# Kernel optimization log

Hardware: AMD Instinct MI355X
Metric: run time of the kernel (lower is better)

The kernel has to match this reference:

```python
import jax, jax.numpy as jnp
import numpy as np

EPSILON = 1e-06
N_TOKENS = 65536
WIDTH_IN = 1024
WIDTH_OUT = 1024
NUM_HEAD = 16
DIM_HEAD = 64


def setup_inputs() -> dict:
    key = jax.random.key(0)
    k_x, k_b, k_lin, k_ker = jax.random.split(key, 4)
    x = jax.random.normal(k_x, (N_TOKENS, WIDTH_IN), dtype=jnp.float32)
    norm_bias = jax.random.normal(k_b, (N_TOKENS, NUM_HEAD, DIM_HEAD), dtype=jnp.float32)
    # LinearLayer: std = 1/sqrt(width_in), shape (width_in, num_head*dim_head)
    w_lin = jax.random.normal(k_lin, (WIDTH_IN, NUM_HEAD * DIM_HEAD), dtype=jnp.float32) / np.sqrt(WIDTH_IN)
    # Grouped kernel: (num_head, dim_head, width_out // num_head), scaled 1/sqrt(dim_head)
    kernel = jax.random.normal(k_ker, (NUM_HEAD, DIM_HEAD, WIDTH_OUT // NUM_HEAD), dtype=jnp.float32) / np.sqrt(DIM_HEAD)
    return {"x": x, "norm_bias": norm_bias, "w_lin": w_lin, "kernel": kernel}


def reference(x, norm_bias, w_lin, kernel):
    # Dense projection, bias-free
    xx = x @ w_lin                                   # [N, H*D]
    xx = xx.reshape(*x.shape[:-1], NUM_HEAD, DIM_HEAD)  # [N, H, D]
    # Per-head RMSNorm
    xx = xx / jnp.sqrt(jnp.mean(jnp.square(xx), axis=-1, keepdims=True) + EPSILON)
    # Optional norm-bias blend
    xx = (xx + norm_bias.reshape(xx.shape)) / 2 ** 0.5
    # Per-head grouped matmul
    xx = jnp.einsum('nhd,hdf->nhf', xx, kernel)      # [N, H, F]
    return xx.reshape(*x.shape[:-1], -1)             # [N, H*F]
```

## Files before the change

### kernel.cpp

```cpp
#include <hip/hip_runtime.h>


typedef __attribute__((ext_vector_type(8))) __bf16 bf16x8;
typedef __attribute__((ext_vector_type(4))) float f32x4;
typedef __attribute__((ext_vector_type(8))) unsigned short ushort8;

__device__ __forceinline__ unsigned short f2bf(float f) {
  unsigned int u = __builtin_bit_cast(unsigned int, f);
  u += 0x7FFFu + ((u >> 16) & 1u);
  return (unsigned short)(u >> 16);
}

__device__ __forceinline__ f32x4 mfma_bf16(bf16x8 a, bf16x8 b, f32x4 c) {
  return __builtin_amdgcn_mfma_f32_16x16x32_bf16(a, b, c, 0, 0, 0);
}

__device__ __forceinline__ void gl_lds16(const void* g, void* l) {
  __builtin_amdgcn_global_load_lds(
      (const __attribute__((address_space(1))) unsigned int*)g,
      (__attribute__((address_space(3))) unsigned int*)l, 16, 0, 0);
}

__global__ void prep_w(const float* __restrict__ w, unsigned short* __restrict__ wb) {
  const int kg = blockIdx.x, ct = blockIdx.y, col = threadIdx.x;
  const int n = ct * 128 + col;
  ushort8 v;
  #pragma unroll
  for (int j = 0; j < 8; ++j) v[j] = f2bf(w[(size_t)(kg * 8 + j) * 1024 + n]);
  *reinterpret_cast<ushort8*>(wb + ((size_t)(ct * 128 + kg) * 128 + col) * 8) = v;
}

__global__ void transpose_k(const float* __restrict__ kin, unsigned short* __restrict__ kt) {
  __shared__ float tile[64][65];
  const int h = blockIdx.x;
  const int t = threadIdx.x;
  #pragma unroll
  for (int i = 0; i < 16; ++i) {
    int idx = i * 256 + t;
    tile[idx >> 6][idx & 63] = kin[(size_t)h * 4096 + idx];
  }
  __syncthreads();
  #pragma unroll
  for (int i = 0; i < 16; ++i) {
    int idx = i * 256 + t;
    kt[(size_t)h * 4096 + idx] = f2bf(tile[idx & 63][idx >> 6]);
  }
}

__global__ __launch_bounds__(256, 3)
void fused_main(const float* __restrict__ x,
                const float* __restrict__ nbias,
                const unsigned short* __restrict__ wb,
                const unsigned short* __restrict__ kt,
                float* __restrict__ out)
{
  __shared__ __align__(16) unsigned char smem[49152];
  const int tid  = threadIdx.x;
  const int wv   = tid >> 6, lane = tid & 63;
  const int l15  = lane & 15, lg = lane >> 4;
  const int wr   = wv >> 1, wc = wv & 1;

  const int bid  = blockIdx.x;
  const int gx   = bid & 7, slot = bid >> 3;
  const int rt   = ((slot >> 3) << 3) + gx;
  const int ct   = slot & 7;
  const size_t row0 = (size_t)rt * 128;

  const float* xb = x + row0 * 1024;
  const unsigned short* wbase = wb + (size_t)ct * 131072;

  f32x4 acc[4][4];
  const f32x4 z4 = {0.f, 0.f, 0.f, 0.f};
  #pragma unroll
  for (int mi = 0; mi < 4; ++mi)
    #pragma unroll
    for (int ni = 0; ni < 4; ++ni) acc[mi][ni] = z4;

  auto stageA = [&](int t, unsigned char* Ab) {
    #pragma unroll
    for (int it = 0; it < 4; ++it) {
      const int L = it * 4096 + tid * 16;
      const int row = L >> 7;
      const int off = (L & 127) ^ ((row & 7) << 4);
      gl_lds16(xb + (size_t)row * 1024 + t * 32 + (off >> 2), Ab + L);
    }
  };
  auto stageB = [&](int t, unsigned char* Bb) {
    #pragma unroll
    for (int it = 0; it < 2; ++it) {
      const int L = it * 4096 + tid * 16;
      gl_lds16(wbase + t * 4096 + (L >> 1), Bb + L);
    }
  };

  stageA(0, smem);
  stageB(0, smem + 32768);

  for (int t = 0; t < 32; ++t) {
    __syncthreads();
    const int nb = (t + 1) & 1;
    if (t < 31) {
      stageA(t + 1, smem + (nb << 14));
      stageB(t + 1, smem + 32768 + (nb << 13));
    }
    const unsigned char* A = smem + ((t & 1) << 14);
    const unsigned char* B = smem + 32768 + ((t & 1) << 13);

    bf16x8 af[4], bfr[4];
    #pragma unroll
    for (int mi = 0; mi < 4; ++mi) {
      const int row = wr * 64 + mi * 16 + l15;
      const int base = row * 128 + ((lg * 32) ^ ((row & 7) << 4));
      f32x4 lo = *reinterpret_cast<const f32x4*>(A + base);
      f32x4 hi = *reinterpret_cast<const f32x4*>(A + (base ^ 16));
      bf16x8 a;
      #pragma unroll
      for (int j = 0; j < 4; ++j) { a[j] = (__bf16)lo[j]; a[4 + j] = (__bf16)hi[j]; }
      af[mi] = a;
    }
    #pragma unroll
    for (int ni = 0; ni < 4; ++ni) {
      const int col = wc * 64 + ni * 16 + l15;
      bfr[ni] = *reinterpret_cast<const bf16x8*>(B + lg * 2048 + col * 16);
    }
    #pragma unroll
    for (int mi = 0; mi < 4; ++mi)
      #pragma unroll
      for (int ni = 0; ni < 4; ++ni)
        acc[mi][ni] = mfma_bf16(af[mi], bfr[ni], acc[mi][ni]);
  }

  __syncthreads();

  const int h = ct * 2 + wc;
  unsigned short* yw = reinterpret_cast<unsigned short*>(smem) + wv * 5120;
  const float* bb = nbias + (row0 + wr * 64) * 1024 + (size_t)h * 64 + l15;

  #pragma unroll
  for (int mi = 0; mi < 4; ++mi) {
    float ss[4];
    #pragma unroll
    for (int r = 0; r < 4; ++r) {
      float p = 0.f;
      #pragma unroll
      for (int ni = 0; ni < 4; ++ni) { const float v = acc[mi][ni][r]; p += v * v; }
      ss[r] = p;
    }
    #pragma unroll
    for (int s = 1; s < 16; s <<= 1)
      #pragma unroll
      for (int r = 0; r < 4; ++r) ss[r] += __shfl_xor(ss[r], s, 64);
    #pragma unroll
    for (int r = 0; r < 4; ++r) {
      const float rs = rsqrtf(ss[r] * 0.015625f + 1e-6f);
      const int rl = mi * 16 + lg * 4 + r;
      const float* bp = bb + (size_t)rl * 1024;
      #pragma unroll
      for (int ni = 0; ni < 4; ++ni) {
        const float y = (acc[mi][ni][r] * rs + bp[ni * 16]) * 0.70710678118654752f;
        __bf16 yb = (__bf16)y;
        yw[rl * 80 + ni * 16 + l15] = __builtin_bit_cast(unsigned short, yb);
      }
    }
  }

  const unsigned short* ktp = kt + (size_t)h * 4096;
  bf16x8 b2[4][2];
  #pragma unroll
  for (int ff = 0; ff < 4; ++ff)
    #pragma unroll
    for (int ks = 0; ks < 2; ++ks)
      b2[ff][ks] = *reinterpret_cast<const bf16x8*>(ktp + (ff * 16 + l15) * 64 + ks * 32 + 8 * lg);

  #pragma unroll
  for (int m2 = 0; m2 < 4; ++m2) {
    f32x4 a2[4] = {z4, z4, z4, z4};
    #pragma unroll
    for (int ks = 0; ks < 2; ++ks) {
      bf16x8 a = *reinterpret_cast<const bf16x8*>(yw + (m2 * 16 + l15) * 80 + ks * 32 + 8 * lg);
      #pragma unroll
      for (int ff = 0; ff < 4; ++ff) a2[ff] = mfma_bf16(a, b2[ff][ks], a2[ff]);
    }
    float* ob = out + (row0 + wr * 64 + m2 * 16 + lg * 4) * 1024 + ct * 128 + wc * 64 + l15;
    #pragma unroll
    for (int ff = 0; ff < 4; ++ff)
      #pragma unroll
      for (int r = 0; r < 4; ++r)
        ob[(size_t)r * 1024 + ff * 16] = a2[ff][r];
  }
}

extern "C" void kernel_launch(void* const* d_in, const int* in_sizes, int n_in,
                              void* d_out, int out_size, void* d_ws, size_t ws_size,
                              hipStream_t stream) {
  const float* x  = (const float*)d_in[0];
  const float* nb = (const float*)d_in[1];
  const float* wl = (const float*)d_in[2];
  const float* kr = (const float*)d_in[3];
  float* out = (float*)d_out;

  unsigned short* wbp = (unsigned short*)d_ws;
  unsigned short* ktp = wbp + 1024 * 1024;

  hipLaunchKernelGGL(prep_w, dim3(128, 8), dim3(128), 0, stream, wl, wbp);
  hipLaunchKernelGGL(transpose_k, dim3(16), dim3(256), 0, stream, kr, ktp);
  hipLaunchKernelGGL(fused_main, dim3(4096), dim3(256), 0, stream, x, nb, wbp, ktp, out);
}
```

Before: 291.7 us.

## Stage A through registers as bf16 with K=64 tiles and explicit pipelining

The main GEMM loop now loads x tiles into registers two steps ahead and converts them to bf16 before writing them to LDS. Before, fp32 went straight to LDS and each step converted it again. K tiles double to 64 (16 iterations), weights are repacked to match, and explicit waitcnt/sched_barrier control overlaps the loads with the MFMA phases. LDS grows to 64KB and occupancy drops to 2 blocks per CU. The epilogue staging buffer uses an XOR swizzle instead of padding to avoid bank conflicts. The cost is higher register pressure from prefetch registers and lower occupancy.

New measurement: 301.4 us. +3.3%, slower.

```diff
diff --git a/kernel.cpp b/kernel.cpp
--- a/kernel.cpp
+++ b/kernel.cpp
@@ -3,6 +3,7 @@
 
 typedef __attribute__((ext_vector_type(8))) __bf16 bf16x8;
 typedef __attribute__((ext_vector_type(4))) float f32x4;
+typedef __attribute__((ext_vector_type(2))) unsigned int uint2v;
 typedef __attribute__((ext_vector_type(8))) unsigned short ushort8;
 
 __device__ __forceinline__ unsigned short f2bf(float f) {
@@ -21,13 +22,18 @@
       (__attribute__((address_space(3))) unsigned int*)l, 16, 0, 0);
 }
 
-__global__ void prep_w(const float* __restrict__ w, unsigned short* __restrict__ wb) {
-  const int kg = blockIdx.x, ct = blockIdx.y, col = threadIdx.x;
-  const int n = ct * 128 + col;
-  ushort8 v;
-  #pragma unroll
-  for (int j = 0; j < 8; ++j) v[j] = f2bf(w[(size_t)(kg * 8 + j) * 1024 + n]);
-  *reinterpret_cast<ushort8*>(wb + ((size_t)(ct * 128 + kg) * 128 + col) * 8) = v;
+__global__ void prep_w2(const float* __restrict__ w, unsigned short* __restrict__ wb) {
+  const int kt = blockIdx.x, ct = blockIdx.y, col = threadIdx.x;
+  #pragma unroll
+  for (int kc = 0; kc < 8; ++kc) {
+    ushort8 v;
+    #pragma unroll
+    for (int j = 0; j < 8; ++j) {
+      const int k = kt * 64 + (kc >> 2) * 32 + (kc & 3) * 8 + j;
+      v[j] = f2bf(w[(size_t)k * 1024 + ct * 128 + col]);
+    }
+    *reinterpret_cast<ushort8*>(wb + ((((size_t)ct * 16 + kt) * 8 + kc) * 128 + col) * 8) = v;
+  }
 }
 
 __global__ void transpose_k(const float* __restrict__ kin, unsigned short* __restrict__ kt) {
@@ -47,27 +53,35 @@
   }
 }
 
-__global__ __launch_bounds__(256, 3)
+__global__ __launch_bounds__(256, 2)
 void fused_main(const float* __restrict__ x,
                 const float* __restrict__ nbias,
                 const unsigned short* __restrict__ wb,
-                const unsigned short* __restrict__ kt,
+                const unsigned short* __restrict__ ktg,
                 float* __restrict__ out)
 {
-  __shared__ __align__(16) unsigned char smem[49152];
-  const int tid  = threadIdx.x;
-  const int wv   = tid >> 6, lane = tid & 63;
-  const int l15  = lane & 15, lg = lane >> 4;
-  const int wr   = wv >> 1, wc = wv & 1;
-
-  const int bid  = blockIdx.x;
-  const int gx   = bid & 7, slot = bid >> 3;
-  const int rt   = ((slot >> 3) << 3) + gx;
-  const int ct   = slot & 7;
+  __shared__ __align__(16) unsigned char smem[65536];
+  const int tid = threadIdx.x;
+  const int wv = tid >> 6, lane = tid & 63, l15 = lane & 15, lg = lane >> 4;
+  const int wr = wv >> 1, wc = wv & 1;
+  const int bid = blockIdx.x;
+  const int gx = bid & 7, slot = bid >> 3;
+  const int rt = ((slot >> 3) << 3) + gx;
+  const int ct = slot & 7;
   const size_t row0 = (size_t)rt * 128;
 
   const float* xb = x + row0 * 1024;
-  const unsigned short* wbase = wb + (size_t)ct * 131072;
+  const unsigned char* wsrc = reinterpret_cast<const unsigned char*>(wb) + (size_t)ct * 262144;
+
+  const int ar_ = tid >> 4, ac_ = tid & 15;
+  const float* agp = xb + (size_t)ar_ * 1024 + ac_ * 4;
+  const int aw_off = (ac_ * 8) ^ ((ar_ & 7) << 4);
+
+  const int abase = (wr * 64 + l15) * 128;
+  const int aswz  = (l15 & 7) << 4;
+  const int ofs0  = (lg * 16) ^ aswz;
+  const int ofs1  = (64 + lg * 16) ^ aswz;
+  const int bcol  = (wc * 64 + l15) * 16 + lg * 2048;
 
   f32x4 acc[4][4];
   const f32x4 z4 = {0.f, 0.f, 0.f, 0.f};
@@ -76,64 +90,89 @@
     #pragma unroll
     for (int ni = 0; ni < 4; ++ni) acc[mi][ni] = z4;
 
-  auto stageA = [&](int t, unsigned char* Ab) {
+  f32x4 arg[2][8];
+
+  auto stageB = [&](int t, int bsel) {
+    unsigned char* Bb = smem + 32768 + (bsel << 14);
     #pragma unroll
     for (int it = 0; it < 4; ++it) {
       const int L = it * 4096 + tid * 16;
-      const int row = L >> 7;
-      const int off = (L & 127) ^ ((row & 7) << 4);
-      gl_lds16(xb + (size_t)row * 1024 + t * 32 + (off >> 2), Ab + L);
-    }
-  };
-  auto stageB = [&](int t, unsigned char* Bb) {
-    #pragma unroll
-    for (int it = 0; it < 2; ++it) {
-      const int L = it * 4096 + tid * 16;
-      gl_lds16(wbase + t * 4096 + (L >> 1), Bb + L);
-    }
-  };
-
-  stageA(0, smem);
-  stageB(0, smem + 32768);
-
-  for (int t = 0; t < 32; ++t) {
-    __syncthreads();
-    const int nb = (t + 1) & 1;
-    if (t < 31) {
-      stageA(t + 1, smem + (nb << 14));
-      stageB(t + 1, smem + 32768 + (nb << 13));
-    }
-    const unsigned char* A = smem + ((t & 1) << 14);
-    const unsigned char* B = smem + 32768 + ((t & 1) << 13);
-
-    bf16x8 af[4], bfr[4];
-    #pragma unroll
-    for (int mi = 0; mi < 4; ++mi) {
-      const int row = wr * 64 + mi * 16 + l15;
-      const int base = row * 128 + ((lg * 32) ^ ((row & 7) << 4));
-      f32x4 lo = *reinterpret_cast<const f32x4*>(A + base);
-      f32x4 hi = *reinterpret_cast<const f32x4*>(A + (base ^ 16));
-      bf16x8 a;
-      #pragma unroll
-      for (int j = 0; j < 4; ++j) { a[j] = (__bf16)lo[j]; a[4 + j] = (__bf16)hi[j]; }
-      af[mi] = a;
-    }
-    #pragma unroll
-    for (int ni = 0; ni < 4; ++ni) {
-      const int col = wc * 64 + ni * 16 + l15;
-      bfr[ni] = *reinterpret_cast<const bf16x8*>(B + lg * 2048 + col * 16);
-    }
+      gl_lds16(wsrc + (size_t)t * 16384 + L, Bb + L);
+    }
+  };
+  auto loadA = [&](int t, f32x4* dst) {
+    #pragma unroll
+    for (int j = 0; j < 8; ++j)
+      dst[j] = *reinterpret_cast<const f32x4*>(agp + j * 16384 + t * 64);
+  };
+  auto cvtwrA = [&](const f32x4* src, int bsel) {
+    unsigned char* Ab = smem + (bsel << 14);
+    #pragma unroll
+    for (int j = 0; j < 8; ++j) {
+      const f32x4 v = src[j];
+      unsigned int lo = ((unsigned)__builtin_bit_cast(unsigned short, (__bf16)v[0])) |
+                        ((unsigned)__builtin_bit_cast(unsigned short, (__bf16)v[1]) << 16);
+      unsigned int hi = ((unsigned)__builtin_bit_cast(unsigned short, (__bf16)v[2])) |
+                        ((unsigned)__builtin_bit_cast(unsigned short, (__bf16)v[3]) << 16);
+      uint2v p; p[0] = lo; p[1] = hi;
+      *reinterpret_cast<uint2v*>(Ab + j * 2048 + ar_ * 128 + aw_off) = p;
+    }
+  };
+  auto phase = [&](int csel, int ks) {
+    const unsigned char* Ab = smem + (csel << 14);
+    const unsigned char* Bb = smem + 32768 + (csel << 14);
+    const int aofs = ks ? ofs1 : ofs0;
+    bf16x8 af[4], bq[4];
     #pragma unroll
     for (int mi = 0; mi < 4; ++mi)
+      af[mi] = *reinterpret_cast<const bf16x8*>(Ab + abase + mi * 2048 + aofs);
+    #pragma unroll
+    for (int ni = 0; ni < 4; ++ni)
+      bq[ni] = *reinterpret_cast<const bf16x8*>(Bb + (ks << 13) + bcol + ni * 256);
+    #pragma unroll
+    for (int mi = 0; mi < 4; ++mi)
       #pragma unroll
       for (int ni = 0; ni < 4; ++ni)
-        acc[mi][ni] = mfma_bf16(af[mi], bfr[ni], acc[mi][ni]);
+        acc[mi][ni] = mfma_bf16(af[mi], bq[ni], acc[mi][ni]);
+  };
+
+  stageB(0, 0);
+  __builtin_amdgcn_sched_barrier(0);
+  loadA(0, arg[0]);
+  loadA(1, arg[1]);
+  __builtin_amdgcn_sched_barrier(0);
+  cvtwrA(arg[0], 0);
+  asm volatile("s_waitcnt lgkmcnt(0)" ::: "memory");
+  __builtin_amdgcn_sched_barrier(0);
+  __builtin_amdgcn_s_barrier();
+  __builtin_amdgcn_sched_barrier(0);
+
+  #pragma unroll
+  for (int t = 0; t < 16; ++t) {
+    const int c = t & 1, n = c ^ 1;
+    if (t + 1 < 16) stageB(t + 1, n);
+    __builtin_amdgcn_sched_barrier(0);
+    if (t + 2 < 16) loadA(t + 2, arg[c]);
+    __builtin_amdgcn_sched_barrier(0);
+
+    phase(c, 0);
+    if (t + 1 < 16) cvtwrA(arg[n], n);
+    phase(c, 1);
+
+    if (t + 1 < 16) {
+      asm volatile("s_waitcnt lgkmcnt(0)" ::: "memory");
+      if (t + 2 < 16) asm volatile("s_waitcnt vmcnt(8)" ::: "memory");
+      else            asm volatile("s_waitcnt vmcnt(0)" ::: "memory");
+      __builtin_amdgcn_sched_barrier(0);
+      __builtin_amdgcn_s_barrier();
+      __builtin_amdgcn_sched_barrier(0);
+    }
   }
 
   __syncthreads();
 
   const int h = ct * 2 + wc;
-  unsigned short* yw = reinterpret_cast<unsigned short*>(smem) + wv * 5120;
+  unsigned short* yw = reinterpret_cast<unsigned short*>(smem) + wv * 4096;
   const float* bb = nbias + (row0 + wr * 64) * 1024 + (size_t)h * 64 + l15;
 
   #pragma unroll
@@ -158,13 +197,13 @@
       #pragma unroll
       for (int ni = 0; ni < 4; ++ni) {
         const float y = (acc[mi][ni][r] * rs + bp[ni * 16]) * 0.70710678118654752f;
-        __bf16 yb = (__bf16)y;
-        yw[rl * 80 + ni * 16 + l15] = __builtin_bit_cast(unsigned short, yb);
+        const __bf16 yb = (__bf16)y;
+        yw[rl * 64 + ((ni * 16 + l15) ^ ((rl & 7) << 3))] = __builtin_bit_cast(unsigned short, yb);
       }
     }
   }
 
-  const unsigned short* ktp = kt + (size_t)h * 4096;
+  const unsigned short* ktp = ktg + (size_t)h * 4096;
   bf16x8 b2[4][2];
   #pragma unroll
   for (int ff = 0; ff < 4; ++ff)
@@ -175,9 +214,11 @@
   #pragma unroll
   for (int m2 = 0; m2 < 4; ++m2) {
     f32x4 a2[4] = {z4, z4, z4, z4};
+    const int row = m2 * 16 + l15;
     #pragma unroll
     for (int ks = 0; ks < 2; ++ks) {
-      bf16x8 a = *reinterpret_cast<const bf16x8*>(yw + (m2 * 16 + l15) * 80 + ks * 32 + 8 * lg);
+      bf16x8 a = *reinterpret_cast<const bf16x8*>(
+          yw + row * 64 + ((ks * 32 + lg * 8) ^ ((row & 7) << 3)));
       #pragma unroll
       for (int ff = 0; ff < 4; ++ff) a2[ff] = mfma_bf16(a, b2[ff][ks], a2[ff]);
     }
@@ -202,7 +243,7 @@
   unsigned short* wbp = (unsigned short*)d_ws;
   unsigned short* ktp = wbp + 1024 * 1024;
 
-  hipLaunchKernelGGL(prep_w, dim3(128, 8), dim3(128), 0, stream, wl, wbp);
+  hipLaunchKernelGGL(prep_w2, dim3(16, 8), dim3(128), 0, stream, wl, wbp);
   hipLaunchKernelGGL(transpose_k, dim3(16), dim3(256), 0, stream, kr, ktp);
   hipLaunchKernelGGL(fused_main, dim3(4096), dim3(256), 0, stream, x, nb, wbp, ktp, out);
 }
```

## Pre-convert x to bf16 and enlarge tiles to 256x256 with triple-buffered pipeline

Applied to the files above, without the earlier changes.

Adds a separate pass that converts x to bf16 in workspace, processing it in chunks if the workspace is small. The main kernel then streams bf16 A tiles instead of fp32, which halves A traffic and removes per-iteration conversions. The block tile grows to 256x256 with 512 threads and 8x4 MFMA fragments per wave. A three-stage LDS pipeline with explicit vmcnt waits, barriers and setprio, plus swizzled layouts for W and the epilogue buffer, aims to hide load latency. The cost is an extra full read and write of x, higher register pressure and fewer resident blocks.

New measurement: 391.7 us. 1.34x slower.

```diff
diff --git a/kernel.cpp b/kernel.cpp
--- a/kernel.cpp
+++ b/kernel.cpp
@@ -5,29 +5,44 @@
 typedef __attribute__((ext_vector_type(4))) float f32x4;
 typedef __attribute__((ext_vector_type(8))) unsigned short ushort8;
 
-__device__ __forceinline__ unsigned short f2bf(float f) {
-  unsigned int u = __builtin_bit_cast(unsigned int, f);
-  u += 0x7FFFu + ((u >> 16) & 1u);
-  return (unsigned short)(u >> 16);
-}
-
+__device__ __forceinline__ unsigned short bfbits(float f) {
+  return __builtin_bit_cast(unsigned short, (__bf16)f);
+}
 __device__ __forceinline__ f32x4 mfma_bf16(bf16x8 a, bf16x8 b, f32x4 c) {
   return __builtin_amdgcn_mfma_f32_16x16x32_bf16(a, b, c, 0, 0, 0);
 }
-
 __device__ __forceinline__ void gl_lds16(const void* g, void* l) {
   __builtin_amdgcn_global_load_lds(
       (const __attribute__((address_space(1))) unsigned int*)g,
       (__attribute__((address_space(3))) unsigned int*)l, 16, 0, 0);
 }
 
+__global__ void cvt_x(const float* __restrict__ x, unsigned short* __restrict__ xb, int n8) {
+  int i = blockIdx.x * blockDim.x + threadIdx.x;
+  const int stride = gridDim.x * blockDim.x;
+  for (; i < n8; i += stride) {
+    f32x4 a = *reinterpret_cast<const f32x4*>(x + (size_t)i * 8);
+    f32x4 b = *reinterpret_cast<const f32x4*>(x + (size_t)i * 8 + 4);
+    ushort8 v;
+    v[0] = bfbits(a[0]); v[1] = bfbits(a[1]); v[2] = bfbits(a[2]); v[3] = bfbits(a[3]);
+    v[4] = bfbits(b[0]); v[5] = bfbits(b[1]); v[6] = bfbits(b[2]); v[7] = bfbits(b[3]);
+    *reinterpret_cast<ushort8*>(xb + (size_t)i * 8) = v;
+  }
+}
+
 __global__ void prep_w(const float* __restrict__ w, unsigned short* __restrict__ wb) {
-  const int kg = blockIdx.x, ct = blockIdx.y, col = threadIdx.x;
-  const int n = ct * 128 + col;
+  const int g = blockIdx.x * 256 + threadIdx.x;
+  const int ct = g >> 15;
+  const int rem = g & 32767;
+  const int t = rem >> 10;
+  const int c = rem & 1023;
+  const int kh = c >> 9, r = (c >> 1) & 255, s = c & 1;
+  const int col = ct * 256 + r;
+  const int k0 = t * 32 + kh * 16 + ((s ^ ((r >> 2) & 1)) << 3);
   ushort8 v;
   #pragma unroll
-  for (int j = 0; j < 8; ++j) v[j] = f2bf(w[(size_t)(kg * 8 + j) * 1024 + n]);
-  *reinterpret_cast<ushort8*>(wb + ((size_t)(ct * 128 + kg) * 128 + col) * 8) = v;
+  for (int j = 0; j < 8; ++j) v[j] = bfbits(w[(size_t)(k0 + j) * 1024 + col]);
+  *reinterpret_cast<ushort8*>(wb + (size_t)g * 8) = v;
 }
 
 __global__ void transpose_k(const float* __restrict__ kin, unsigned short* __restrict__ kt) {
@@ -43,150 +58,159 @@
   #pragma unroll
   for (int i = 0; i < 16; ++i) {
     int idx = i * 256 + t;
-    kt[(size_t)h * 4096 + idx] = f2bf(tile[idx & 63][idx >> 6]);
-  }
-}
-
-__global__ __launch_bounds__(256, 3)
-void fused_main(const float* __restrict__ x,
+    kt[(size_t)h * 4096 + idx] = bfbits(tile[idx & 63][idx >> 6]);
+  }
+}
+
+__global__ __launch_bounds__(512, 2)
+void fused_main(const unsigned short* __restrict__ xb,
                 const float* __restrict__ nbias,
                 const unsigned short* __restrict__ wb,
-                const unsigned short* __restrict__ kt,
-                float* __restrict__ out)
+                const unsigned short* __restrict__ ktg,
+                float* __restrict__ out,
+                long row0_base, int nb8)
 {
-  __shared__ __align__(16) unsigned char smem[49152];
-  const int tid  = threadIdx.x;
-  const int wv   = tid >> 6, lane = tid & 63;
-  const int l15  = lane & 15, lg = lane >> 4;
-  const int wr   = wv >> 1, wc = wv & 1;
-
-  const int bid  = blockIdx.x;
-  const int gx   = bid & 7, slot = bid >> 3;
-  const int rt   = ((slot >> 3) << 3) + gx;
-  const int ct   = slot & 7;
-  const size_t row0 = (size_t)rt * 128;
-
-  const float* xb = x + row0 * 1024;
-  const unsigned short* wbase = wb + (size_t)ct * 131072;
-
-  f32x4 acc[4][4];
+  __shared__ __align__(16) unsigned char smem[98304];
+  const int tid = threadIdx.x;
+  const int wv = tid >> 6, lane = tid & 63, l15 = lane & 15, lg = lane >> 4;
+  const int wr = wv >> 2, wc = wv & 3;
+  const int bid = blockIdx.x;
+  const int v = (bid & 7) * nb8 + (bid >> 3);
+  const int rt = v >> 2, ct = v & 3;
+  const long grow0 = row0_base + (long)rt * 256;
+  const size_t lrow0 = (size_t)rt * 256;
+
+  const int u = tid;
+  const int sr = u >> 1, ss = u & 1;
+  const int slog = (ss ^ ((sr >> 2) & 1)) << 4;
+  const char* asrc = (const char*)xb + (lrow0 + sr) * 2048 + slog;
+  const char* bsrc = (const char*)wb + (size_t)ct * 524288 + (size_t)u * 16;
+
+  const int fswz = (((lg & 1) ^ ((l15 >> 2) & 1)) << 4);
+  const int aoff = (lg >> 1) * 8192 + (wr * 128 + l15) * 32 + fswz;
+  const int boff = (lg >> 1) * 8192 + (wc * 64 + l15) * 32 + fswz;
+
+  f32x4 acc[8][4];
   const f32x4 z4 = {0.f, 0.f, 0.f, 0.f};
   #pragma unroll
-  for (int mi = 0; mi < 4; ++mi)
+  for (int mi = 0; mi < 8; ++mi)
     #pragma unroll
     for (int ni = 0; ni < 4; ++ni) acc[mi][ni] = z4;
 
-  auto stageA = [&](int t, unsigned char* Ab) {
-    #pragma unroll
-    for (int it = 0; it < 4; ++it) {
-      const int L = it * 4096 + tid * 16;
-      const int row = L >> 7;
-      const int off = (L & 127) ^ ((row & 7) << 4);
-      gl_lds16(xb + (size_t)row * 1024 + t * 32 + (off >> 2), Ab + L);
+  auto stage = [&](int t) {
+    const int b = t % 3;
+    unsigned char* Ab = smem + b * 16384;
+    unsigned char* Bb = smem + 49152 + b * 16384;
+    const char* as = asrc + (size_t)t * 64;
+    const char* bs = bsrc + (size_t)t * 16384;
+    gl_lds16(as,        Ab + u * 16);
+    gl_lds16(as + 32,   Ab + 8192 + u * 16);
+    gl_lds16(bs,        Bb + u * 16);
+    gl_lds16(bs + 8192, Bb + 8192 + u * 16);
+  };
+  auto compute = [&](int t) {
+    const int b = t % 3;
+    const unsigned char* Ab = smem + b * 16384;
+    const unsigned char* Bb = smem + 49152 + b * 16384;
+    bf16x8 af[8], bq[4];
+    #pragma unroll
+    for (int mi = 0; mi < 8; ++mi)
+      af[mi] = *reinterpret_cast<const bf16x8*>(Ab + aoff + mi * 512);
+    #pragma unroll
+    for (int ni = 0; ni < 4; ++ni)
+      bq[ni] = *reinterpret_cast<const bf16x8*>(Bb + boff + ni * 512);
+    __builtin_amdgcn_s_setprio(1);
+    #pragma unroll
+    for (int mi = 0; mi < 8; ++mi)
+      #pragma unroll
+      for (int ni = 0; ni < 4; ++ni)
+        acc[mi][ni] = mfma_bf16(af[mi], bq[ni], acc[mi][ni]);
+    __builtin_amdgcn_s_setprio(0);
+  };
+
+  stage(0); stage(1);
+  asm volatile("s_waitcnt vmcnt(4)" ::: "memory");
+  __builtin_amdgcn_sched_barrier(0);
+  __builtin_amdgcn_s_barrier();
+  __builtin_amdgcn_sched_barrier(0);
+
+  #pragma unroll
+  for (int t = 0; t < 32; ++t) {
+    if (t + 2 < 32) { stage(t + 2); __builtin_amdgcn_sched_barrier(0); }
+    compute(t);
+    if (t < 31) {
+      __builtin_amdgcn_sched_barrier(0);
+      if (t + 2 < 32) asm volatile("s_waitcnt vmcnt(4)" ::: "memory");
+      else            asm volatile("s_waitcnt vmcnt(0)" ::: "memory");
+      __builtin_amdgcn_sched_barrier(0);
+      __builtin_amdgcn_s_barrier();
+      __builtin_amdgcn_sched_barrier(0);
     }
-  };
-  auto stageB = [&](int t, unsigned char* Bb) {
-    #pragma unroll
-    for (int it = 0; it < 2; ++it) {
-      const int L = it * 4096 + tid * 16;
-      gl_lds16(wbase + t * 4096 + (L >> 1), Bb + L);
-    }
-  };
-
-  stageA(0, smem);
-  stageB(0, smem + 32768);
-
-  for (int t = 0; t < 32; ++t) {
-    __syncthreads();
-    const int nb = (t + 1) & 1;
-    if (t < 31) {
-      stageA(t + 1, smem + (nb << 14));
-      stageB(t + 1, smem + 32768 + (nb << 13));
-    }
-    const unsigned char* A = smem + ((t & 1) << 14);
-    const unsigned char* B = smem + 32768 + ((t & 1) << 13);
-
-    bf16x8 af[4], bfr[4];
-    #pragma unroll
-    for (int mi = 0; mi < 4; ++mi) {
-      const int row = wr * 64 + mi * 16 + l15;
-      const int base = row * 128 + ((lg * 32) ^ ((row & 7) << 4));
-      f32x4 lo = *reinterpret_cast<const f32x4*>(A + base);
-      f32x4 hi = *reinterpret_cast<const f32x4*>(A + (base ^ 16));
-      bf16x8 a;
-      #pragma unroll
-      for (int j = 0; j < 4; ++j) { a[j] = (__bf16)lo[j]; a[4 + j] = (__bf16)hi[j]; }
-      af[mi] = a;
-    }
-    #pragma unroll
-    for (int ni = 0; ni < 4; ++ni) {
-      const int col = wc * 64 + ni * 16 + l15;
-      bfr[ni] = *reinterpret_cast<const bf16x8*>(B + lg * 2048 + col * 16);
-    }
-    #pragma unroll
-    for (int mi = 0; mi < 4; ++mi)
-      #pragma unroll
-      for (int ni = 0; ni < 4; ++ni)
-        acc[mi][ni] = mfma_bf16(af[mi], bfr[ni], acc[mi][ni]);
-  }
-
+  }
+  __builtin_amdgcn_sched_barrier(0);
   __syncthreads();
 
-  const int h = ct * 2 + wc;
-  unsigned short* yw = reinterpret_cast<unsigned short*>(smem) + wv * 5120;
-  const float* bb = nbias + (row0 + wr * 64) * 1024 + (size_t)h * 64 + l15;
-
-  #pragma unroll
-  for (int mi = 0; mi < 4; ++mi) {
-    float ss[4];
-    #pragma unroll
-    for (int r = 0; r < 4; ++r) {
-      float p = 0.f;
-      #pragma unroll
-      for (int ni = 0; ni < 4; ++ni) { const float v = acc[mi][ni][r]; p += v * v; }
-      ss[r] = p;
-    }
-    #pragma unroll
-    for (int s = 1; s < 16; s <<= 1)
-      #pragma unroll
-      for (int r = 0; r < 4; ++r) ss[r] += __shfl_xor(ss[r], s, 64);
-    #pragma unroll
-    for (int r = 0; r < 4; ++r) {
-      const float rs = rsqrtf(ss[r] * 0.015625f + 1e-6f);
-      const int rl = mi * 16 + lg * 4 + r;
-      const float* bp = bb + (size_t)rl * 1024;
-      #pragma unroll
-      for (int ni = 0; ni < 4; ++ni) {
-        const float y = (acc[mi][ni][r] * rs + bp[ni * 16]) * 0.70710678118654752f;
-        __bf16 yb = (__bf16)y;
-        yw[rl * 80 + ni * 16 + l15] = __builtin_bit_cast(unsigned short, yb);
+  const int h = ct * 4 + wc;
+  const unsigned short* ktp = ktg + (size_t)h * 4096;
+  bf16x8 b2[4][2];
+  #pragma unroll
+  for (int ff = 0; ff < 4; ++ff)
+    #pragma unroll
+    for (int ks = 0; ks < 2; ++ks)
+      b2[ff][ks] = *reinterpret_cast<const bf16x8*>(ktp + (ff * 16 + l15) * 64 + ks * 32 + lg * 8);
+
+  unsigned char* yw = smem + wv * 8192;
+  const float* bb = nbias + (size_t)(grow0 + wr * 128) * 1024 + h * 64;
+
+  #pragma unroll
+  for (int hf = 0; hf < 2; ++hf) {
+    #pragma unroll
+    for (int mi4 = 0; mi4 < 4; ++mi4) {
+      const int mi = hf * 4 + mi4;
+      float ss4[4];
+      #pragma unroll
+      for (int r = 0; r < 4; ++r) {
+        float p = 0.f;
+        #pragma unroll
+        for (int ni = 0; ni < 4; ++ni) { const float q = acc[mi][ni][r]; p += q * q; }
+        ss4[r] = p;
+      }
+      #pragma unroll
+      for (int s = 1; s < 16; s <<= 1)
+        #pragma unroll
+        for (int r = 0; r < 4; ++r) ss4[r] += __shfl_xor(ss4[r], s, 64);
+      #pragma unroll
+      for (int r = 0; r < 4; ++r) {
+        const float rs = rsqrtf(ss4[r] * 0.015625f + 1e-6f);
+        const int rl = mi4 * 16 + lg * 4 + r;
+        const float* bp = bb + (size_t)(hf * 64 + rl) * 1024;
+        #pragma unroll
+        for (int ni = 0; ni < 4; ++ni) {
+          const float y = (acc[mi][ni][r] * rs + bp[ni * 16 + l15]) * 0.70710678118654752f;
+          const int cb = ((ni * 16 + l15) * 2) ^ ((rl & 7) << 4);
+          *reinterpret_cast<unsigned short*>(yw + rl * 128 + cb) = bfbits(y);
+        }
       }
     }
-  }
-
-  const unsigned short* ktp = kt + (size_t)h * 4096;
-  bf16x8 b2[4][2];
-  #pragma unroll
-  for (int ff = 0; ff < 4; ++ff)
-    #pragma unroll
-    for (int ks = 0; ks < 2; ++ks)
-      b2[ff][ks] = *reinterpret_cast<const bf16x8*>(ktp + (ff * 16 + l15) * 64 + ks * 32 + 8 * lg);
-
-  #pragma unroll
-  for (int m2 = 0; m2 < 4; ++m2) {
-    f32x4 a2[4] = {z4, z4, z4, z4};
-    #pragma unroll
-    for (int ks = 0; ks < 2; ++ks) {
-      bf16x8 a = *reinterpret_cast<const bf16x8*>(yw + (m2 * 16 + l15) * 80 + ks * 32 + 8 * lg);
-      #pragma unroll
-      for (int ff = 0; ff < 4; ++ff) a2[ff] = mfma_bf16(a, b2[ff][ks], a2[ff]);
+    #pragma unroll
+    for (int m2 = 0; m2 < 4; ++m2) {
+      f32x4 a2[4] = {z4, z4, z4, z4};
+      const int row = m2 * 16 + l15;
+      #pragma unroll
+      for (int ks = 0; ks < 2; ++ks) {
+        const int cb = (ks * 64 + lg * 16) ^ ((row & 7) << 4);
+        bf16x8 a = *reinterpret_cast<const bf16x8*>(yw + row * 128 + cb);
+        #pragma unroll
+        for (int ff = 0; ff < 4; ++ff) a2[ff] = mfma_bf16(a, b2[ff][ks], a2[ff]);
+      }
+      float* ob = out + (size_t)(grow0 + wr * 128 + hf * 64 + m2 * 16 + lg * 4) * 1024
+                      + ct * 256 + wc * 64 + l15;
+      #pragma unroll
+      for (int ff = 0; ff < 4; ++ff)
+        #pragma unroll
+        for (int r = 0; r < 4; ++r)
+          ob[(size_t)r * 1024 + ff * 16] = a2[ff][r];
     }
-    float* ob = out + (row0 + wr * 64 + m2 * 16 + lg * 4) * 1024 + ct * 128 + wc * 64 + l15;
-    #pragma unroll
-    for (int ff = 0; ff < 4; ++ff)
-      #pragma unroll
-      for (int r = 0; r < 4; ++r)
-        ob[(size_t)r * 1024 + ff * 16] = a2[ff][r];
   }
 }
 
@@ -199,10 +223,29 @@
   const float* kr = (const float*)d_in[3];
   float* out = (float*)d_out;
 
-  unsigned short* wbp = (unsigned short*)d_ws;
-  unsigned short* ktp = wbp + 1024 * 1024;
-
-  hipLaunchKernelGGL(prep_w, dim3(128, 8), dim3(128), 0, stream, wl, wbp);
-  hipLaunchKernelGGL(transpose_k, dim3(16), dim3(256), 0, stream, kr, ktp);
-  hipLaunchKernelGGL(fused_main, dim3(4096), dim3(256), 0, stream, x, nb, wbp, ktp, out);
-}
+  unsigned short* wb = (unsigned short*)d_ws;
+  unsigned short* kt = wb + 1048576;
+  const size_t xb_off = 2228224;
+  unsigned short* xb = (unsigned short*)((char*)d_ws + xb_off);
+
+  long rows_chunk;
+  if (ws_size >= xb_off + 134217728ull) {
+    rows_chunk = 65536;
+  } else {
+    size_t usable = ws_size > xb_off ? ws_size - xb_off : 0;
+    rows_chunk = (long)(usable / 2048) & ~511L;
+    if (rows_chunk < 512) rows_chunk = 512;
+  }
+
+  hipLaunchKernelGGL(prep_w, dim3(512), dim3(256), 0, stream, wl, wb);
+  hipLaunchKernelGGL(transpose_k, dim3(16), dim3(256), 0, stream, kr, kt);
+
+  for (long r0 = 0; r0 < 65536; r0 += rows_chunk) {
+    const long cr = (65536 - r0 < rows_chunk) ? (65536 - r0) : rows_chunk;
+    hipLaunchKernelGGL(cvt_x, dim3(1024), dim3(256), 0, stream,
+                       x + (size_t)r0 * 1024, xb, (int)(cr * 128));
+    const int nblk = (int)(cr / 256) * 4;
+    hipLaunchKernelGGL(fused_main, dim3(nblk), dim3(512), 0, stream,
+                       xb, nb, wb, kt, out, r0, nblk / 8);
+  }
+}
```
